# Kernel optimization log

Measured on AMD Instinct MI355X. Metric: run time of the kernel, lower is better.

The kernel has to match this reference:

```python
import math
import jax, jax.numpy as jnp
import numpy as np

L = 16
LOG2T = 19
T = 1 << LOG2T
F = 2
N_MIN = 16
N_MAX = 2048
N_PTS = 1048576

# intended geometric growth factor (source has a parenthesization bug)
_B = math.exp((math.log(N_MAX) - math.log(N_MIN)) / (L - 1))
RESOLUTIONS = [int(math.floor(N_MIN * (_B ** i))) for i in range(L)]

# 8 corner offsets of a voxel, [8, 3]
_OFFS_NP = np.stack(np.meshgrid([0, 1], [0, 1], [0, 1], indexing='ij'), -1).reshape(8, 3)
# spatial hash primes from Instant-NGP
_PRIMES_NP = np.array([1, 2654435761, 805459861], dtype=np.uint32)


def setup_inputs() -> dict:
    key = jax.random.key(0)
    k1, k2 = jax.random.split(key)
    x = jax.random.uniform(k1, (N_PTS, 3), dtype=jnp.float32)  # positions in [0,1)
    table = jax.random.normal(k2, (L, T, F), dtype=jnp.float32) * 1e-4
    return {"x": x, "table": table}


def _encode(x, table):
    offs_i = jnp.asarray(_OFFS_NP, dtype=jnp.uint32)          # [8,3]
    offs_f = jnp.asarray(_OFFS_NP, dtype=x.dtype)             # [8,3]
    primes = jnp.asarray(_PRIMES_NP)                          # [3] uint32
    mask = jnp.uint32(T - 1)
    outs = []
    for lvl in range(L):
        res = RESOLUTIONS[lvl]
        xs = x * res                                           # [N,3]
        x0 = jnp.floor(xs)
        w = xs - x0                                            # [N,3] trilerp weights
        # corner integer coords, [N,8,3]
        c = x0.astype(jnp.uint32)[:, None, :] + offs_i[None]
        # spatial hash: xor of coord*prime, masked to T (T is a power of 2)
        hp = c * primes                                        # uint32 wraparound mul
        h = (hp[..., 0] ^ hp[..., 1] ^ hp[..., 2]) & mask      # [N,8]
        feats = table[lvl][h.astype(jnp.int32)]                # [N,8,F] gather
        # trilinear weights: prod over dims of (w if corner==1 else 1-w)
        wts = jnp.prod(jnp.where(offs_f[None] == 1.0, w[:, None, :], 1.0 - w[:, None, :]), axis=-1)  # [N,8]
        outs.append(jnp.einsum('nc,ncf->nf', wts, feats))      # [N,F]
    return jnp.concatenate(outs, axis=-1)                      # [N, L*F]


def reference(x, table):
    return _encode(x, table)
```

## Files before the change

### kernel.cpp

```cpp
#include <hip/hip_runtime.h>
#include <cmath>

#define NPTS   1048576
#define NLVL   16
#define NLOW   5
#define NHEAVY (NLVL - NLOW)
#define T      (1u << 19)
#define TMASK  (T - 1u)
#define P1     2654435761u
#define P2     805459861u

typedef float v2f __attribute__((ext_vector_type(2)));
typedef float v4f __attribute__((ext_vector_type(4)));

struct Corners { uint32_t h[8]; float wt[8]; };

__device__ __forceinline__ Corners mk_corners(float px, float py, float pz, float rf) {
    Corners cc;
    const float xs0 = px * rf, xs1 = py * rf, xs2 = pz * rf;
    const float f0 = floorf(xs0), f1 = floorf(xs1), f2 = floorf(xs2);
    const float w0 = xs0 - f0, w1 = xs1 - f1, w2 = xs2 - f2;
    const uint32_t i0 = (uint32_t)f0, i1 = (uint32_t)f1, i2 = (uint32_t)f2;
    const uint32_t A0 = i0,      A1 = i0 + 1u;
    const uint32_t B0 = i1 * P1, B1 = B0 + P1;
    const uint32_t C0 = i2 * P2, C1 = C0 + P2;
    cc.h[0] = (A0 ^ B0 ^ C0) & TMASK;  cc.h[1] = (A0 ^ B0 ^ C1) & TMASK;
    cc.h[2] = (A0 ^ B1 ^ C0) & TMASK;  cc.h[3] = (A0 ^ B1 ^ C1) & TMASK;
    cc.h[4] = (A1 ^ B0 ^ C0) & TMASK;  cc.h[5] = (A1 ^ B0 ^ C1) & TMASK;
    cc.h[6] = (A1 ^ B1 ^ C0) & TMASK;  cc.h[7] = (A1 ^ B1 ^ C1) & TMASK;
    const float u0 = 1.0f - w0, u1 = 1.0f - w1, u2 = 1.0f - w2;
    cc.wt[0] = (u0 * u1) * u2;  cc.wt[1] = (u0 * u1) * w2;
    cc.wt[2] = (u0 * w1) * u2;  cc.wt[3] = (u0 * w1) * w2;
    cc.wt[4] = (w0 * u1) * u2;  cc.wt[5] = (w0 * u1) * w2;
    cc.wt[6] = (w0 * w1) * u2;  cc.wt[7] = (w0 * w1) * w2;
    return cc;
}

__global__ __launch_bounds__(256) void hashgrid_lvl2pt(
    const float* __restrict__ x,
    const float* __restrict__ tb,
    float* __restrict__ wsl,
    float rf)
{
    const int t  = blockIdx.x * 256 + threadIdx.x;
    const int n0 = t;
    const int n1 = t + NPTS / 2;

    const float p0x = __builtin_nontemporal_load(x + 3 * (size_t)n0 + 0);
    const float p0y = __builtin_nontemporal_load(x + 3 * (size_t)n0 + 1);
    const float p0z = __builtin_nontemporal_load(x + 3 * (size_t)n0 + 2);
    const float p1x = __builtin_nontemporal_load(x + 3 * (size_t)n1 + 0);
    const float p1y = __builtin_nontemporal_load(x + 3 * (size_t)n1 + 1);
    const float p1z = __builtin_nontemporal_load(x + 3 * (size_t)n1 + 2);

    const Corners c0 = mk_corners(p0x, p0y, p0z, rf);
    const Corners c1 = mk_corners(p1x, p1y, p1z, rf);

    float a00 = 0.f, a01 = 0.f, a10 = 0.f, a11 = 0.f;
#pragma unroll
    for (int c = 0; c < 8; ++c) {
        const float2 g0 = *(const float2*)(tb + 2 * (size_t)c0.h[c]);
        const float2 g1 = *(const float2*)(tb + 2 * (size_t)c1.h[c]);
        a00 += c0.wt[c] * g0.x;  a01 += c0.wt[c] * g0.y;
        a10 += c1.wt[c] * g1.x;  a11 += c1.wt[c] * g1.y;
    }
    v2f r0; r0.x = a00; r0.y = a01;
    v2f r1; r1.x = a10; r1.y = a11;
    __builtin_nontemporal_store(r0, (v2f*)(wsl + (size_t)n0 * 2));
    __builtin_nontemporal_store(r1, (v2f*)(wsl + (size_t)n1 * 2));
}

__global__ __launch_bounds__(256) void hashgrid_final(
    const float* __restrict__ x,
    const float* __restrict__ table,
    const float* __restrict__ ws,
    float* __restrict__ out,
    float r0, float r1, float r2, float r3, float r4)
{
    const int n = blockIdx.x * 256 + threadIdx.x;
    float acc[2 * NLVL];

#pragma unroll
    for (int j = 0; j < NHEAVY; ++j) {
        const v2f g = __builtin_nontemporal_load(
            (const v2f*)(ws + ((size_t)j << 21) + (size_t)n * 2));
        acc[2 * (NLOW + j) + 0] = g.x;
        acc[2 * (NLOW + j) + 1] = g.y;
    }

    const float px = __builtin_nontemporal_load(x + 3 * (size_t)n + 0);
    const float py = __builtin_nontemporal_load(x + 3 * (size_t)n + 1);
    const float pz = __builtin_nontemporal_load(x + 3 * (size_t)n + 2);

    const float rs[NLOW] = {r0, r1, r2, r3, r4};
#pragma unroll
    for (int l = 0; l < NLOW; ++l) {
        const Corners cc = mk_corners(px, py, pz, rs[l]);
        const float* tb = table + ((size_t)l << 20);
        float a0 = 0.f, a1 = 0.f;
#pragma unroll
        for (int c = 0; c < 8; ++c) {
            const float2 g = *(const float2*)(tb + 2 * (size_t)cc.h[c]);
            a0 += cc.wt[c] * g.x;
            a1 += cc.wt[c] * g.y;
        }
        acc[2 * l + 0] = a0;
        acc[2 * l + 1] = a1;
    }

    v4f* op = (v4f*)(out + (size_t)n * 32);
#pragma unroll
    for (int k = 0; k < 8; ++k) {
        v4f v; v.x = acc[4*k]; v.y = acc[4*k+1]; v.z = acc[4*k+2]; v.w = acc[4*k+3];
        op[k] = v;
    }
}

__global__ __launch_bounds__(256) void hashgrid_lvl_direct(
    const float* __restrict__ x,
    const float* __restrict__ tb,
    float* __restrict__ outl,
    float rf)
{
    const int n = blockIdx.x * 256 + threadIdx.x;
    const float px = __builtin_nontemporal_load(x + 3 * (size_t)n + 0);
    const float py = __builtin_nontemporal_load(x + 3 * (size_t)n + 1);
    const float pz = __builtin_nontemporal_load(x + 3 * (size_t)n + 2);
    const Corners cc = mk_corners(px, py, pz, rf);
    float a0 = 0.f, a1 = 0.f;
#pragma unroll
    for (int c = 0; c < 8; ++c) {
        const float2 g = *(const float2*)(tb + 2 * (size_t)cc.h[c]);
        a0 += cc.wt[c] * g.x;
        a1 += cc.wt[c] * g.y;
    }
    outl[(size_t)n * 32 + 0] = a0;
    outl[(size_t)n * 32 + 1] = a1;
}

extern "C" void kernel_launch(void* const* d_in, const int* in_sizes, int n_in,
                              void* d_out, int out_size, void* d_ws, size_t ws_size,
                              hipStream_t stream) {
    const float* x     = (const float*)d_in[0];
    const float* table = (const float*)d_in[1];
    float* out         = (float*)d_out;
    float* ws          = (float*)d_ws;

    double (*volatile p_log)(double)          = log;
    double (*volatile p_exp)(double)          = exp;
    double (*volatile p_pow)(double, double)  = pow;
    double (*volatile p_floor)(double)        = floor;

    const double b = p_exp((p_log(2048.0) - p_log(16.0)) / 15.0);
    float rf[NLVL];
    for (int l = 0; l < NLVL; ++l)
        rf[l] = (float)(int)p_floor(16.0 * p_pow(b, (double)l));

    const bool use_ws = ws_size >= (size_t)NHEAVY * NPTS * 2 * sizeof(float);

    if (!use_ws) {
        for (int l = 0; l < NLVL; ++l)
            hashgrid_lvl_direct<<<NPTS / 256, 256, 0, stream>>>(
                x, table + ((size_t)l << 20), out + 2 * l, rf[l]);
        return;
    }

    for (int l = NLOW; l < NLVL; ++l) {
        hashgrid_lvl2pt<<<NPTS / 512, 256, 0, stream>>>(
            x, table + ((size_t)l << 20), ws + ((size_t)(l - NLOW) << 21), rf[l]);
    }
    hashgrid_final<<<NPTS / 256, 256, 0, stream>>>(
        x, table, ws, out, rf[0], rf[1], rf[2], rf[3], rf[4]);
}
```

Measured before the change: 564.4 us.

## Split low levels into per-level kernels and process 4 points per thread

Heavy hash levels now handle four points per thread instead of two, so more gathers are in flight per thread. The five low-resolution levels move out of the final kernel into their own per-level kernels that write to workspace. A pure transpose kernel then gathers all 16 levels into the output. This aims to raise memory-level parallelism and keep each kernel working on a single table level for cache locality. In exchange it needs a larger workspace, adds five more launches, and adds extra workspace write and read traffic for the low levels.

```diff
diff --git a/kernel.cpp b/kernel.cpp
--- a/kernel.cpp
+++ b/kernel.cpp
@@ -4,7 +4,6 @@
 #define NPTS   1048576
 #define NLVL   16
 #define NLOW   5
-#define NHEAVY (NLVL - NLOW)
 #define T      (1u << 19)
 #define TMASK  (T - 1u)
 #define P1     2654435761u
@@ -36,78 +35,74 @@
     return cc;
 }
 
-__global__ __launch_bounds__(256) void hashgrid_lvl2pt(
+__global__ __launch_bounds__(256) void hashgrid_lvl1(
     const float* __restrict__ x,
     const float* __restrict__ tb,
     float* __restrict__ wsl,
     float rf)
 {
-    const int t  = blockIdx.x * 256 + threadIdx.x;
-    const int n0 = t;
-    const int n1 = t + NPTS / 2;
-
-    const float p0x = __builtin_nontemporal_load(x + 3 * (size_t)n0 + 0);
-    const float p0y = __builtin_nontemporal_load(x + 3 * (size_t)n0 + 1);
-    const float p0z = __builtin_nontemporal_load(x + 3 * (size_t)n0 + 2);
-    const float p1x = __builtin_nontemporal_load(x + 3 * (size_t)n1 + 0);
-    const float p1y = __builtin_nontemporal_load(x + 3 * (size_t)n1 + 1);
-    const float p1z = __builtin_nontemporal_load(x + 3 * (size_t)n1 + 2);
-
-    const Corners c0 = mk_corners(p0x, p0y, p0z, rf);
-    const Corners c1 = mk_corners(p1x, p1y, p1z, rf);
-
-    float a00 = 0.f, a01 = 0.f, a10 = 0.f, a11 = 0.f;
+    const int n = blockIdx.x * 256 + threadIdx.x;
+    const float px = __builtin_nontemporal_load(x + 3 * (size_t)n + 0);
+    const float py = __builtin_nontemporal_load(x + 3 * (size_t)n + 1);
+    const float pz = __builtin_nontemporal_load(x + 3 * (size_t)n + 2);
+    const Corners cc = mk_corners(px, py, pz, rf);
+    float a0 = 0.f, a1 = 0.f;
 #pragma unroll
     for (int c = 0; c < 8; ++c) {
-        const float2 g0 = *(const float2*)(tb + 2 * (size_t)c0.h[c]);
-        const float2 g1 = *(const float2*)(tb + 2 * (size_t)c1.h[c]);
-        a00 += c0.wt[c] * g0.x;  a01 += c0.wt[c] * g0.y;
-        a10 += c1.wt[c] * g1.x;  a11 += c1.wt[c] * g1.y;
+        const float2 g = *(const float2*)(tb + 2 * (size_t)cc.h[c]);
+        a0 += cc.wt[c] * g.x;
+        a1 += cc.wt[c] * g.y;
     }
-    v2f r0; r0.x = a00; r0.y = a01;
-    v2f r1; r1.x = a10; r1.y = a11;
-    __builtin_nontemporal_store(r0, (v2f*)(wsl + (size_t)n0 * 2));
-    __builtin_nontemporal_store(r1, (v2f*)(wsl + (size_t)n1 * 2));
+    v2f r; r.x = a0; r.y = a1;
+    __builtin_nontemporal_store(r, (v2f*)(wsl + (size_t)n * 2));
 }
 
-__global__ __launch_bounds__(256) void hashgrid_final(
+__global__ __launch_bounds__(256) void hashgrid_lvl4pt(
     const float* __restrict__ x,
-    const float* __restrict__ table,
+    const float* __restrict__ tb,
+    float* __restrict__ wsl,
+    float rf)
+{
+    const int t = blockIdx.x * 256 + threadIdx.x;
+
+    float a0[4], a1[4];
+#pragma unroll
+    for (int p = 0; p < 4; ++p) {
+        const int n = t + p * (NPTS / 4);
+        const float px = __builtin_nontemporal_load(x + 3 * (size_t)n + 0);
+        const float py = __builtin_nontemporal_load(x + 3 * (size_t)n + 1);
+        const float pz = __builtin_nontemporal_load(x + 3 * (size_t)n + 2);
+        const Corners cc = mk_corners(px, py, pz, rf);
+        float s0 = 0.f, s1 = 0.f;
+#pragma unroll
+        for (int c = 0; c < 8; ++c) {
+            const float2 g = *(const float2*)(tb + 2 * (size_t)cc.h[c]);
+            s0 += cc.wt[c] * g.x;
+            s1 += cc.wt[c] * g.y;
+        }
+        a0[p] = s0; a1[p] = s1;
+    }
+#pragma unroll
+    for (int p = 0; p < 4; ++p) {
+        const int n = t + p * (NPTS / 4);
+        v2f r; r.x = a0[p]; r.y = a1[p];
+        __builtin_nontemporal_store(r, (v2f*)(wsl + (size_t)n * 2));
+    }
+}
+
+__global__ __launch_bounds__(256) void hashgrid_transpose(
     const float* __restrict__ ws,
-    float* __restrict__ out,
-    float r0, float r1, float r2, float r3, float r4)
+    float* __restrict__ out)
 {
     const int n = blockIdx.x * 256 + threadIdx.x;
     float acc[2 * NLVL];
-
 #pragma unroll
-    for (int j = 0; j < NHEAVY; ++j) {
+    for (int l = 0; l < NLVL; ++l) {
         const v2f g = __builtin_nontemporal_load(
-            (const v2f*)(ws + ((size_t)j << 21) + (size_t)n * 2));
-        acc[2 * (NLOW + j) + 0] = g.x;
-        acc[2 * (NLOW + j) + 1] = g.y;
+            (const v2f*)(ws + ((size_t)l << 21) + (size_t)n * 2));
+        acc[2 * l + 0] = g.x;
+        acc[2 * l + 1] = g.y;
     }
-
-    const float px = __builtin_nontemporal_load(x + 3 * (size_t)n + 0);
-    const float py = __builtin_nontemporal_load(x + 3 * (size_t)n + 1);
-    const float pz = __builtin_nontemporal_load(x + 3 * (size_t)n + 2);
-
-    const float rs[NLOW] = {r0, r1, r2, r3, r4};
-#pragma unroll
-    for (int l = 0; l < NLOW; ++l) {
-        const Corners cc = mk_corners(px, py, pz, rs[l]);
-        const float* tb = table + ((size_t)l << 20);
-        float a0 = 0.f, a1 = 0.f;
-#pragma unroll
-        for (int c = 0; c < 8; ++c) {
-            const float2 g = *(const float2*)(tb + 2 * (size_t)cc.h[c]);
-            a0 += cc.wt[c] * g.x;
-            a1 += cc.wt[c] * g.y;
-        }
-        acc[2 * l + 0] = a0;
-        acc[2 * l + 1] = a1;
-    }
-
     v4f* op = (v4f*)(out + (size_t)n * 32);
 #pragma unroll
     for (int k = 0; k < 8; ++k) {
@@ -156,7 +151,7 @@
     for (int l = 0; l < NLVL; ++l)
         rf[l] = (float)(int)p_floor(16.0 * p_pow(b, (double)l));
 
-    const bool use_ws = ws_size >= (size_t)NHEAVY * NPTS * 2 * sizeof(float);
+    const bool use_ws = ws_size >= (size_t)NLVL * NPTS * 2 * sizeof(float);
 
     if (!use_ws) {
         for (int l = 0; l < NLVL; ++l)
@@ -166,9 +161,12 @@
     }
 
     for (int l = NLOW; l < NLVL; ++l) {
-        hashgrid_lvl2pt<<<NPTS / 512, 256, 0, stream>>>(
-            x, table + ((size_t)l << 20), ws + ((size_t)(l - NLOW) << 21), rf[l]);
+        hashgrid_lvl4pt<<<NPTS / 1024, 256, 0, stream>>>(
+            x, table + ((size_t)l << 20), ws + ((size_t)l << 21), rf[l]);
     }
-    hashgrid_final<<<NPTS / 256, 256, 0, stream>>>(
-        x, table, ws, out, rf[0], rf[1], rf[2], rf[3], rf[4]);
+    for (int l = 0; l < NLOW; ++l) {
+        hashgrid_lvl1<<<NPTS / 256, 256, 0, stream>>>(
+            x, table + ((size_t)l << 20), ws + ((size_t)l << 21), rf[l]);
+    }
+    hashgrid_transpose<<<NPTS / 256, 256, 0, stream>>>(ws, out);
 }
```

New measurement: 623.7 us. +10.5%, slower.
